# Kernel optimization log

Hardware: AMD Instinct MI355X
Metric: run time of the kernel (lower is better)

The kernel has to match this reference:

```python
import jax, jax.numpy as jnp
import numpy as np

B, C, H, W = 1, 192, 96, 96


def setup_inputs() -> dict:
    key = jax.random.key(0)
    k1, k2 = jax.random.split(key, 2)
    latent_feats = jax.random.normal(k1, (B, C, H, W), dtype=jnp.float32)
    refined_feats = jax.random.normal(k2, (B, C, H, W), dtype=jnp.float32)
    w_4 = jnp.ones((1, C, H, W), dtype=jnp.float32)
    w_5 = jnp.ones((1, C, H, W), dtype=jnp.float32)
    return {"latent_feats": latent_feats, "refined_feats": refined_feats, "w_4": w_4, "w_5": w_5}


def reference(latent_feats, refined_feats, w_4, w_5):
    # b == 1 (torch.mm requires 2D operands, so the original only works for batch 1)
    hw = H * W
    lat = (latent_feats * w_4)[0].reshape(C, hw)          # [c, hw]
    ref = refined_feats[0].reshape(C, hw)                 # [c, hw]
    scores = jnp.einsum('cn,cm->nm', ref, lat)            # [(hw)_ref, (hw)_lat]
    attn = jax.nn.softmax(scores, axis=-2)                # softmax over rows (dim -2)
    ctx = jnp.einsum('cn,nm->cm', lat, attn)              # [c, hw]
    return refined_feats * w_5 + ctx.reshape(1, C, H, W)
```

## Files before the change

kernel.cpp:

```cpp
#include <hip/hip_runtime.h>
#include <stdint.h>


#define NQ 9216
#define NC 192
#define FR 1769472
#define LOG2E 1.4426950408889634f
#define M0L 36.06737602f

typedef short    bfrag  __attribute__((ext_vector_type(8)));
typedef _Float16 hfrag  __attribute__((ext_vector_type(8)));
typedef short    sfrag4 __attribute__((ext_vector_type(4)));
typedef float    facc16 __attribute__((ext_vector_type(16)));

__device__ __forceinline__ short f2bf(float x) {
    uint32_t u = __builtin_bit_cast(uint32_t, x);
    u = (u + 0x7fffu + ((u >> 16) & 1u)) >> 16;
    return (short)u;
}
__device__ __forceinline__ float bf2f(short s) {
    uint32_t u = ((uint32_t)(uint16_t)s) << 16;
    return __builtin_bit_cast(float, u);
}
__device__ __forceinline__ int cvtpk_bf16(float lo, float hi) {
    int r;
    asm("v_cvt_pk_bf16_f32 %0, %1, %2" : "=v"(r) : "v"(lo), "v"(hi));
    return r;
}
__device__ __forceinline__ float exp2_raw(float x) {
    float r;
    asm("v_exp_f32 %0, %1" : "=v"(r) : "v"(x));
    return r;
}
__device__ __forceinline__ bfrag words_to_frag(int w0, int w1, int w2, int w3) {
    union { int i[4]; bfrag f; } u;
    u.i[0] = w0; u.i[1] = w1; u.i[2] = w2; u.i[3] = w3;
    return u.f;
}
__device__ __forceinline__ void gload_lds16(const void* g, void* l) {
    __builtin_amdgcn_global_load_lds(
        (__attribute__((address_space(1))) const void*)(uintptr_t)g,
        (__attribute__((address_space(3))) void*)(uint32_t)(uintptr_t)l,
        16, 0, 0);
}

__global__ __launch_bounds__(256) void InterGate_prep(
    const float* __restrict__ latent, const float* __restrict__ refined,
    const float* __restrict__ w4,
    short* __restrict__ Qf, short* __restrict__ KV)
{
    const int wid  = blockIdx.x * 4 + (threadIdx.x >> 6);
    const int lane = threadIdx.x & 63;
    const int l32  = lane & 31, h = lane >> 5;

    if (wid < 3456) {
        const int qw = wid / 12, t = wid % 12;
        const int q  = qw * 32 + l32;
        const int c0 = t * 16 + h * 8;
        hfrag hv;
        #pragma unroll
        for (int i = 0; i < 8; i++) {
            size_t idx = (size_t)(c0 + i) * NQ + q;
            hv[i] = (_Float16)(latent[idx] * w4[idx] * LOG2E);
        }
        *(hfrag*)(void*)(Qf + ((size_t)wid * 64 + lane) * 8) = hv;
    } else if (wid < 6912) {
        const int u = wid - 3456;
        const int g = u / 12, t = u % 12;
        const int key = g * 32 + l32;
        const int c0  = t * 16 + h * 8;
        hfrag hv;
        #pragma unroll
        for (int i = 0; i < 8; i++) {
            size_t idx = (size_t)(c0 + i) * NQ + key;
            hv[i] = (_Float16)refined[idx];
        }
        *(hfrag*)(void*)(KV + (size_t)g * 12288 + ((t * 64 + lane) * 8)) = hv;
    } else {
        const int u = wid - 6912;
        const int g = u / 12, r = u % 12;
        const int T = r / 6, cb = r % 6;
        const int c  = cb * 32 + l32;
        const int k0 = g * 32 + T * 16 + 4 * h;
        bfrag bv;
        #pragma unroll
        for (int i = 0; i < 8; i++) {
            const int row = k0 + (i & 3) + 8 * (i >> 2);
            size_t idx = (size_t)c * NQ + row;
            bv[i] = f2bf(latent[idx] * w4[idx]);
        }
        *(bfrag*)(void*)(KV + (size_t)g * 12288 + 6144 + ((T * 6 + cb) * 64 + lane) * 8) = bv;
    }
}

__device__ __forceinline__ void stage24(const short* KV, int g, char* dstb,
                                        int w, int lane) {
    const char* src = (const char*)(KV + (size_t)g * 12288) + w * 6144 + lane * 16;
    char* dst = dstb + w * 6144;
    #pragma unroll
    for (int j = 0; j < 6; j++) gload_lds16(src + j * 1024, dst + j * 1024);
}

__global__ __launch_bounds__(256, 2) void InterGate_flash(
    const short* __restrict__ Qf, const short* __restrict__ KV,
    short* __restrict__ Opart, float* __restrict__ l_ws, int KS)
{
    __shared__ __align__(16) short kv[3][12288];

    const int tid  = threadIdx.x;
    const int lane = tid & 63, w = tid >> 6;
    const int l32  = lane & 31, h = lane >> 5;
    const int qt   = blockIdx.x, ks = blockIdx.y;

    const int base = 288 / KS, rem = 288 % KS;
    const int start = ks * base + (ks < rem ? ks : rem);
    const int cnt   = base + (ks < rem ? 1 : 0);

    const int qw = qt * 4 + w;
    hfrag qf[12];
    #pragma unroll
    for (int t = 0; t < 12; t++)
        qf[t] = *(const hfrag*)(const void*)(Qf + (((size_t)qw * 12 + t) * 64 + lane) * 8);

    facc16 O[6];
    #pragma unroll
    for (int cb = 0; cb < 6; cb++)
        #pragma unroll
        for (int j = 0; j < 16; j++) O[cb][j] = 0.f;
    float lsum = 0.f;

    stage24(KV, start, (char*)&kv[0][0], w, lane);
    if (cnt > 1) stage24(KV, start + 1, (char*)&kv[1][0], w, lane);

    int bufc = 0;
    for (int kt = 0; kt < cnt; kt++) {
        if (kt + 1 < cnt) { asm volatile("s_waitcnt vmcnt(6)" ::: "memory"); }
        else              { asm volatile("s_waitcnt vmcnt(0)" ::: "memory"); }
        __builtin_amdgcn_s_barrier();

        const short* kb = &kv[bufc][0];
        const int bufn = bufc + 2 >= 3 ? bufc - 1 : bufc + 2;
        if (kt + 2 < cnt)
            stage24(KV, start + kt + 2, (char*)&kv[bufn][0], w, lane);

        facc16 S;
        #pragma unroll
        for (int j = 0; j < 16; j++) S[j] = 0.f;
        __builtin_amdgcn_s_setprio(1);
        #pragma unroll
        for (int t = 0; t < 12; t++) {
            hfrag kf = *(const hfrag*)(const void*)(kb + t * 512 + lane * 8);
            S = __builtin_amdgcn_mfma_f32_32x32x16_f16(kf, qf[t], S, 0, 0, 0);
        }
        __builtin_amdgcn_s_setprio(0);

        float p[16];
        #pragma unroll
        for (int j = 0; j < 16; j++) p[j] = exp2_raw(S[j] - M0L);
        lsum += (((p[0]+p[1])+(p[2]+p[3]))+((p[4]+p[5])+(p[6]+p[7])))
              + (((p[8]+p[9])+(p[10]+p[11]))+((p[12]+p[13])+(p[14]+p[15])));
        int cp[8];
        #pragma unroll
        for (int a = 0; a < 8; a++) cp[a] = cvtpk_bf16(p[2 * a], p[2 * a + 1]);

        #pragma unroll
        for (int T = 0; T < 2; T++) {
            bfrag pf = words_to_frag(cp[4*T], cp[4*T+1], cp[4*T+2], cp[4*T+3]);
            __builtin_amdgcn_s_setprio(1);
            #pragma unroll
            for (int cb = 0; cb < 6; cb++) {
                bfrag vf = *(const bfrag*)(const void*)(kb + 6144 + (T * 6 + cb) * 512 + lane * 8);
                O[cb] = __builtin_amdgcn_mfma_f32_32x32x16_bf16(vf, pf, O[cb], 0, 0, 0);
            }
            __builtin_amdgcn_s_setprio(0);
        }
        bufc = bufc + 1 >= 3 ? 0 : bufc + 1;
    }

    const int q0 = qt * 128 + w * 32 + l32;
    short* row = Opart + ((size_t)ks * NQ + q0) * NC;
    #pragma unroll
    for (int cb = 0; cb < 6; cb++) {
        #pragma unroll
        for (int g = 0; g < 4; g++) {
            const int c0 = cb * 32 + 8 * g + 4 * h;
            sfrag4 s4;
            #pragma unroll
            for (int r = 0; r < 4; r++) s4[r] = f2bf(O[cb][4 * g + r]);
            *(sfrag4*)(void*)(row + c0) = s4;
        }
    }
    float lt = lsum + __shfl_xor(lsum, 32);
    if (h == 0) l_ws[(size_t)ks * NQ + q0] = lt;
}

__global__ __launch_bounds__(256) void InterGate_combine(
    const short* __restrict__ Opart, const float* __restrict__ l_ws,
    const float* __restrict__ refined, const float* __restrict__ w5,
    float* __restrict__ out, int KS)
{
    __shared__ float ctx[32][193];
    __shared__ float sInv[32];
    const int qt = blockIdx.x, tid = threadIdx.x;

    if (tid < 32) {
        const int q = qt * 32 + tid;
        float L = 0.f;
        for (int ks = 0; ks < KS; ks++) L += l_ws[(size_t)ks * NQ + q];
        sInv[tid] = 1.f / L;
    }
    __syncthreads();

    for (int u = tid; u < 768; u += 256) {
        const int ql = u / 24, c0 = (u % 24) * 8;
        float acc[8] = {0.f, 0.f, 0.f, 0.f, 0.f, 0.f, 0.f, 0.f};
        for (int ks = 0; ks < KS; ks++) {
            bfrag pk = *(const bfrag*)(const void*)&Opart[((size_t)ks * NQ + qt * 32 + ql) * NC + c0];
            #pragma unroll
            for (int j = 0; j < 8; j++) acc[j] += bf2f(pk[j]);
        }
        const float inv = sInv[ql];
        #pragma unroll
        for (int j = 0; j < 8; j++) ctx[ql][c0 + j] = acc[j] * inv;
    }
    __syncthreads();

    for (int u = tid; u < 6144; u += 256) {
        const int c = u / 32, qx = u % 32;
        size_t o = (size_t)c * NQ + qt * 32 + qx;
        out[o] = refined[o] * w5[o] + ctx[qx][c];
    }
}

extern "C" void kernel_launch(void* const* d_in, const int* in_sizes, int n_in,
                              void* d_out, int out_size, void* d_ws, size_t ws_size,
                              hipStream_t stream)
{
    (void)in_sizes; (void)n_in; (void)out_size;
    const float* latent  = (const float*)d_in[0];
    const float* refined = (const float*)d_in[1];
    const float* w4      = (const float*)d_in[2];
    const float* w5      = (const float*)d_in[3];
    float* out = (float*)d_out;

    short* Qf = (short*)d_ws;
    short* KV = Qf + FR;
    const size_t basebytes = (size_t)3 * FR * 2;

    const int opts[4] = {7, 4, 2, 1};
    int KS = 0;
    for (int i = 0; i < 4; i++) {
        size_t need = basebytes + (size_t)opts[i] * ((size_t)NQ * NC * 2 + (size_t)NQ * 4);
        if (need <= ws_size) { KS = opts[i]; break; }
    }
    if (KS == 0) return;

    short* Opart = (short*)((char*)d_ws + basebytes);
    float* l_ws  = (float*)((char*)d_ws + basebytes + (size_t)KS * NQ * NC * 2);

    InterGate_prep<<<2592, 256, 0, stream>>>(latent, refined, w4, Qf, KV);
    dim3 fg(72, KS);
    InterGate_flash<<<fg, 256, 0, stream>>>(Qf, KV, Opart, l_ws, KS);
    InterGate_combine<<<288, 256, 0, stream>>>(Opart, l_ws, refined, w5, out, KS);
}
```

Measured before the change: 98.30 us.

## Software-pipeline QK and PV MFMAs across key tiles with split K/V buffers

Splits the shared-memory staging into separate K and V triple buffers and restructures the loop so the QK^T MFMAs for tile kt interleave with the PV MFMAs for tile kt-1. The exp/convert for the previous scores no longer sits between the two matmul phases of the same tile, and MFMA work from independent chains can overlap. The change adds a prologue and epilogue, an extra live score accumulator (more registers), and more complex vmcnt accounting that must match the new load counts.

Result: no change. 99.57 us (+1.3%).

```diff
diff --git a/kernel.cpp b/kernel.cpp
--- a/kernel.cpp
+++ b/kernel.cpp
@@ -93,19 +93,20 @@
     }
 }
 
-__device__ __forceinline__ void stage24(const short* KV, int g, char* dstb,
+__device__ __forceinline__ void stage12(const short* KVsrc, char* dstb,
                                         int w, int lane) {
-    const char* src = (const char*)(KV + (size_t)g * 12288) + w * 6144 + lane * 16;
-    char* dst = dstb + w * 6144;
-    #pragma unroll
-    for (int j = 0; j < 6; j++) gload_lds16(src + j * 1024, dst + j * 1024);
+    const char* src = (const char*)KVsrc + w * 3072 + lane * 16;
+    char* dst = dstb + w * 3072;
+    #pragma unroll
+    for (int j = 0; j < 3; j++) gload_lds16(src + j * 1024, dst + j * 1024);
 }
 
 __global__ __launch_bounds__(256, 2) void InterGate_flash(
     const short* __restrict__ Qf, const short* __restrict__ KV,
     short* __restrict__ Opart, float* __restrict__ l_ws, int KS)
 {
-    __shared__ __align__(16) short kv[3][12288];
+    __shared__ __align__(16) short kbufs[3][6144];
+    __shared__ __align__(16) short vbufs[3][6144];
 
     const int tid  = threadIdx.x;
     const int lane = tid & 63, w = tid >> 6;
@@ -129,20 +130,56 @@
         for (int j = 0; j < 16; j++) O[cb][j] = 0.f;
     float lsum = 0.f;
 
-    stage24(KV, start, (char*)&kv[0][0], w, lane);
-    if (cnt > 1) stage24(KV, start + 1, (char*)&kv[1][0], w, lane);
-
-    int bufc = 0;
+    stage12(KV + (size_t)start * 12288,        (char*)&kbufs[0][0], w, lane);
+    stage12(KV + (size_t)start * 12288 + 6144, (char*)&vbufs[0][0], w, lane);
+    if (cnt > 1)
+        stage12(KV + (size_t)(start + 1) * 12288, (char*)&kbufs[1][0], w, lane);
+
+    facc16 Sp;
+    #pragma unroll
+    for (int j = 0; j < 16; j++) Sp[j] = 0.f;
+
     for (int kt = 0; kt < cnt; kt++) {
         if (kt + 1 < cnt) { asm volatile("s_waitcnt vmcnt(6)" ::: "memory"); }
-        else              { asm volatile("s_waitcnt vmcnt(0)" ::: "memory"); }
+        else              { asm volatile("s_waitcnt vmcnt(3)" ::: "memory"); }
         __builtin_amdgcn_s_barrier();
 
-        const short* kb = &kv[bufc][0];
-        const int bufn = bufc + 2 >= 3 ? bufc - 1 : bufc + 2;
         if (kt + 2 < cnt)
-            stage24(KV, start + kt + 2, (char*)&kv[bufn][0], w, lane);
-
+            stage12(KV + (size_t)(start + kt + 2) * 12288,
+                    (char*)&kbufs[(kt + 2) % 3][0], w, lane);
+        if (kt + 1 < cnt)
+            stage12(KV + (size_t)(start + kt + 1) * 12288 + 6144,
+                    (char*)&vbufs[(kt + 1) % 3][0], w, lane);
+
+        const short* kb = &kbufs[kt % 3][0];
+
+        if (kt == 0) {
+            facc16 S;
+            #pragma unroll
+            for (int j = 0; j < 16; j++) S[j] = 0.f;
+            __builtin_amdgcn_s_setprio(1);
+            #pragma unroll
+            for (int t = 0; t < 12; t++) {
+                hfrag kf = *(const hfrag*)(const void*)(kb + t * 512 + lane * 8);
+                S = __builtin_amdgcn_mfma_f32_32x32x16_f16(kf, qf[t], S, 0, 0, 0);
+            }
+            __builtin_amdgcn_s_setprio(0);
+            Sp = S;
+            continue;
+        }
+
+        float p[16];
+        #pragma unroll
+        for (int j = 0; j < 16; j++) p[j] = exp2_raw(Sp[j] - M0L);
+        lsum += (((p[0]+p[1])+(p[2]+p[3]))+((p[4]+p[5])+(p[6]+p[7])))
+              + (((p[8]+p[9])+(p[10]+p[11]))+((p[12]+p[13])+(p[14]+p[15])));
+        int cp[8];
+        #pragma unroll
+        for (int a = 0; a < 8; a++) cp[a] = cvtpk_bf16(p[2 * a], p[2 * a + 1]);
+        bfrag pf0 = words_to_frag(cp[0], cp[1], cp[2], cp[3]);
+        bfrag pf1 = words_to_frag(cp[4], cp[5], cp[6], cp[7]);
+
+        const short* vb = &vbufs[(kt - 1) % 3][0];
         facc16 S;
         #pragma unroll
         for (int j = 0; j < 16; j++) S[j] = 0.f;
@@ -151,30 +188,36 @@
         for (int t = 0; t < 12; t++) {
             hfrag kf = *(const hfrag*)(const void*)(kb + t * 512 + lane * 8);
             S = __builtin_amdgcn_mfma_f32_32x32x16_f16(kf, qf[t], S, 0, 0, 0);
+            bfrag vf = *(const bfrag*)(const void*)(vb + t * 512 + lane * 8);
+            O[t % 6] = __builtin_amdgcn_mfma_f32_32x32x16_bf16(
+                vf, (t < 6 ? pf0 : pf1), O[t % 6], 0, 0, 0);
         }
         __builtin_amdgcn_s_setprio(0);
-
+        Sp = S;
+    }
+
+    asm volatile("s_waitcnt vmcnt(0)" ::: "memory");
+    __builtin_amdgcn_s_barrier();
+    {
         float p[16];
         #pragma unroll
-        for (int j = 0; j < 16; j++) p[j] = exp2_raw(S[j] - M0L);
+        for (int j = 0; j < 16; j++) p[j] = exp2_raw(Sp[j] - M0L);
         lsum += (((p[0]+p[1])+(p[2]+p[3]))+((p[4]+p[5])+(p[6]+p[7])))
               + (((p[8]+p[9])+(p[10]+p[11]))+((p[12]+p[13])+(p[14]+p[15])));
         int cp[8];
         #pragma unroll
         for (int a = 0; a < 8; a++) cp[a] = cvtpk_bf16(p[2 * a], p[2 * a + 1]);
-
-        #pragma unroll
-        for (int T = 0; T < 2; T++) {
-            bfrag pf = words_to_frag(cp[4*T], cp[4*T+1], cp[4*T+2], cp[4*T+3]);
-            __builtin_amdgcn_s_setprio(1);
-            #pragma unroll
-            for (int cb = 0; cb < 6; cb++) {
-                bfrag vf = *(const bfrag*)(const void*)(kb + 6144 + (T * 6 + cb) * 512 + lane * 8);
-                O[cb] = __builtin_amdgcn_mfma_f32_32x32x16_bf16(vf, pf, O[cb], 0, 0, 0);
-            }
-            __builtin_amdgcn_s_setprio(0);
-        }
-        bufc = bufc + 1 >= 3 ? 0 : bufc + 1;
+        bfrag pf0 = words_to_frag(cp[0], cp[1], cp[2], cp[3]);
+        bfrag pf1 = words_to_frag(cp[4], cp[5], cp[6], cp[7]);
+        const short* vb = &vbufs[(cnt - 1) % 3][0];
+        __builtin_amdgcn_s_setprio(1);
+        #pragma unroll
+        for (int t = 0; t < 12; t++) {
+            bfrag vf = *(const bfrag*)(const void*)(vb + t * 512 + lane * 8);
+            O[t % 6] = __builtin_amdgcn_mfma_f32_32x32x16_bf16(
+                vf, (t < 6 ? pf0 : pf1), O[t % 6], 0, 0, 0);
+        }
+        __builtin_amdgcn_s_setprio(0);
     }
 
     const int q0 = qt * 128 + w * 32 + l32;
```
